# Kernel optimization log

Hardware: AMD Instinct MI355X
Metric: run time of the kernel (lower is better)

## Reference

```python
import jax, jax.numpy as jnp
import numpy as np
from jax import lax

VOL_RANGE = (-40.0, -40.0, -1.0, 40.0, 40.0, 5.4)
VOXEL_SIZE = 0.4
GRID_SHAPE = (200, 200, 16)  # int((hi-lo)/voxel_size) per axis
G = 1024                     # number of gaussians
C = 17                       # feature channels (semantic classes)
MAHA_THRESH = 7.5


def _make_grid_coords():
    # generate_grid(grid_shape, offset=0.5) * voxel_size + vol_range[:3]
    axes = [(jnp.arange(GRID_SHAPE[i], dtype=jnp.float32) + 0.5) * VOXEL_SIZE + VOL_RANGE[i]
            for i in range(3)]
    gx, gy, gz = jnp.meshgrid(*axes, indexing='ij')
    return jnp.stack([gx, gy, gz], axis=-1).reshape(-1, 3)  # [N, 3]


def _quat_to_rotmat(q):
    # q: [..., 4] (w, x, y, z), assumed normalized
    w, x, y, z = q[..., 0], q[..., 1], q[..., 2], q[..., 3]
    R = jnp.stack([
        1 - 2 * (y * y + z * z), 2 * (x * y - w * z), 2 * (x * z + w * y),
        2 * (x * y + w * z), 1 - 2 * (x * x + z * z), 2 * (y * z - w * x),
        2 * (x * z - w * y), 2 * (y * z + w * x), 1 - 2 * (x * x + y * y),
    ], axis=-1)
    return R.reshape(*q.shape[:-1], 3, 3)


def setup_inputs() -> dict:
    key = jax.random.key(0)
    k1, k2, k3, k4, k5 = jax.random.split(key, 5)
    lo = jnp.asarray(VOL_RANGE[:3], dtype=jnp.float32)
    hi = jnp.asarray(VOL_RANGE[3:], dtype=jnp.float32)
    means3d = lo + (hi - lo) * jax.random.uniform(k1, (1, G, 3), dtype=jnp.float32)
    opacities = jax.random.uniform(k2, (1, G, 1), dtype=jnp.float32)
    features = jax.random.normal(k3, (1, G, C), dtype=jnp.float32)
    # SPD covariances: R diag(s^2) R^T with realistic ~1m scales
    quats = jax.random.normal(k4, (1, G, 4), dtype=jnp.float32)
    quats = quats / jnp.linalg.norm(quats, axis=-1, keepdims=True)
    R = _quat_to_rotmat(quats)                                   # [1, G, 3, 3]
    scales = 0.5 + jax.random.uniform(k5, (1, G, 3), dtype=jnp.float32)  # in [0.5, 1.5] m
    covariances = jnp.einsum('bgij,bgj,bgkj->bgik', R, scales ** 2, R)
    return {
        'grid_coords': _make_grid_coords(),
        'means3d': means3d,
        'opacities': opacities,
        'features': features,
        'covariances': covariances,
    }


def _splat_one_batch(coords, means, ops, feats, covs):
    # coords: [N, 3]; means: [G, 3]; ops: [G]; feats: [G, C]; covs: [G, 3, 3]
    N = coords.shape[0]
    c = feats.shape[-1]
    inv_covs = jnp.linalg.inv(covs)  # [G, 3, 3]

    def step(carry, inp):
        dsum, fsum, cnt = carry
        mu, A, op, ft = inp
        diff = coords - mu                                  # [N, 3]
        maha = jnp.einsum('ni,ij,nj->n', diff, A, diff)     # [N]
        mask = maha <= MAHA_THRESH
        w = jnp.where(mask, op * jnp.exp(-0.5 * maha), 0.0)  # density contribution
        mf = mask.astype(coords.dtype)
        dsum = dsum + w
        fsum = fsum + mf[:, None] * (op * ft)[None, :]       # feature contribution
        cnt = cnt + mf
        return (dsum, fsum, cnt), None

    init = (jnp.zeros((N,), coords.dtype),
            jnp.zeros((N, c), coords.dtype),
            jnp.zeros((N,), coords.dtype))
    (dsum, fsum, cnt), _ = lax.scan(step, init, (means, inv_covs, ops, feats))
    # running-mean update in the torch loop == masked mean over gaussians
    denom = jnp.maximum(cnt, 1.0)
    return dsum / denom, fsum / denom[:, None]


def reference(grid_coords, means3d, opacities, features, covariances):
    dens, fts = jax.vmap(_splat_one_batch, in_axes=(None, 0, 0, 0, 0))(
        grid_coords, means3d, opacities[..., 0], features, covariances)
    B = means3d.shape[0]
    dens = dens.reshape(B, *GRID_SHAPE, 1)
    fts = fts.reshape(B, *GRID_SHAPE, features.shape[-1])
    return dens, fts
```

## Files before the change

### kernel.cpp

```cpp
#include <hip/hip_runtime.h>
#include <math.h>

#define G_N 1024
#define C_N 17
#define NX 200
#define NY 200
#define NZ 16
#define N_VOX (NX * NY * NZ)
#define MAHA_T 7.5f
#define CAP 128

__launch_bounds__(256, 2)
__global__ void gv_fused_kernel(const float* __restrict__ means,
                                const float* __restrict__ ops,
                                const float* __restrict__ feats,
                                const float* __restrict__ covs,
                                float* __restrict__ dens_out,
                                float* __restrict__ feat_out) {
    __shared__ __align__(16) char smemA[4 * 64 * C_N * 4];
    __shared__ unsigned short s_list[G_N];
    __shared__ int s_wcnt[4];

    const int tid = threadIdx.x;
    const int wave = tid >> 6;
    const int lane = tid & 63;
    const int bx = blockIdx.x, by = blockIdx.y;

    const float x0 = -40.f + (float)(bx * 8) * 0.4f;
    const float x1 = x0 + 3.2f;
    const float y0 = -40.f + (float)(by * 8) * 0.4f;
    const float y1 = y0 + 3.2f;

    unsigned short* s_stage = (unsigned short*)smemA;
    int base = 0;
#pragma unroll
    for (int r = 0; r < 4; ++r) {
        int g = wave * 256 + r * 64 + lane;
        float mx = means[3 * g], my = means[3 * g + 1], mz = means[3 * g + 2];
        float c00 = covs[9 * g], c11 = covs[9 * g + 4], c22 = covs[9 * g + 8];
        float hx = sqrtf(MAHA_T * c00) * 1.01f + 0.01f;
        float hy = sqrtf(MAHA_T * c11) * 1.01f + 0.01f;
        float hz = sqrtf(MAHA_T * c22) * 1.01f + 0.01f;
        bool hit = (mx - hx <= x1) && (mx + hx >= x0) &&
                   (my - hy <= y1) && (my + hy >= y0) &&
                   (mz - hz <= 5.4f) && (mz + hz >= -1.0f);
        unsigned long long m = __ballot(hit);
        int rank = __popcll(m & ((1ull << lane) - 1ull));
        if (hit) s_stage[wave * 256 + base + rank] = (unsigned short)g;
        base += __popcll(m);
    }
    if (lane == 0) s_wcnt[wave] = base;
    __syncthreads();
    const int c0 = s_wcnt[0], c1 = s_wcnt[1], c2 = s_wcnt[2], c3 = s_wcnt[3];
    const int total = c0 + c1 + c2 + c3;
    int off = 0;
    if (wave > 0) off += c0;
    if (wave > 1) off += c1;
    if (wave > 2) off += c2;
    for (int i = lane; i < base; i += 64)
        s_list[off + i] = s_stage[wave * 256 + i];

    const int z = lane & 15;
    const int yv = lane >> 4;
    const int X0 = bx * 8 + 2 * wave;
    const int X1 = X0 + 1;
    const int Ya = by * 8 + yv;

    float cx0, cx1, cya, cyb, cz;
    {
#pragma clang fp contract(off)
        cx0 = ((float)X0 + 0.5f) * 0.4f + -40.0f;
        cx1 = ((float)X1 + 0.5f) * 0.4f + -40.0f;
        cya = ((float)Ya + 0.5f) * 0.4f + -40.0f;
        cyb = ((float)(Ya + 4) + 0.5f) * 0.4f + -40.0f;
        cz  = ((float)z + 0.5f) * 0.4f + -1.0f;
    }

    float dsa = 0.f, dsb = 0.f, dsc = 0.f, dsd = 0.f;
    float cna = 0.f, cnb = 0.f, cnc = 0.f, cnd = 0.f;
    float fa[C_N], fb[C_N], fc[C_N], fd[C_N];
#pragma unroll
    for (int c = 0; c < C_N; ++c) { fa[c] = 0.f; fb[c] = 0.f; fc[c] = 0.f; fd[c] = 0.f; }

#define ACC(F, DS, CN, MH) { DS = fmaf(q0.w, __expf(-0.5f * (MH)), DS); CN += 1.f; \
    F[0] += q2.z;  F[1] += q2.w;  F[2] += q3.x;  F[3] += q3.y;  F[4] += q3.z; \
    F[5] += q3.w;  F[6] += q4.x;  F[7] += q4.y;  F[8] += q4.z;  F[9] += q4.w; \
    F[10] += q5.x; F[11] += q5.y; F[12] += q5.z; F[13] += q5.w; F[14] += q6.x; \
    F[15] += q6.y; F[16] += q6.z; }

    float4* s_gd = (float4*)smemA;
    for (int cb = 0; cb < total; cb += CAP) {
        const int nc = min(CAP, total - cb);
        __syncthreads();
        if (tid < nc) {
            int g = (int)s_list[cb + tid];
            const float* cv = covs + g * 9;
            double c00 = cv[0], c01 = cv[1], c02 = cv[2];
            double c11 = cv[4], c12 = cv[5], c22 = cv[8];
            double m00 = c11 * c22 - c12 * c12;
            double m01 = c02 * c12 - c01 * c22;
            double m02 = c01 * c12 - c02 * c11;
            double det = c00 * m00 + c01 * m01 + c02 * m02;
            double inv = 1.0 / det;
            float a00 = (float)(m00 * inv);
            float a01 = (float)(m01 * inv);
            float a02 = (float)(m02 * inv);
            float a11 = (float)((c00 * c22 - c02 * c02) * inv);
            float a12 = (float)((c02 * c01 - c00 * c12) * inv);
            float a22 = (float)((c00 * c11 - c01 * c01) * inv);
            float mx = means[3 * g], my = means[3 * g + 1], mz = means[3 * g + 2];
            float op = ops[g];
            const float* ft = feats + g * C_N;
            float4* o = s_gd + tid * 7;
            o[0] = make_float4(mx, my, mz, op);
            o[1] = make_float4(a00, a11, a22, 2.f * a01);
            o[2] = make_float4(2.f * a02, 2.f * a12, op * ft[0], op * ft[1]);
            o[3] = make_float4(op * ft[2], op * ft[3], op * ft[4], op * ft[5]);
            o[4] = make_float4(op * ft[6], op * ft[7], op * ft[8], op * ft[9]);
            o[5] = make_float4(op * ft[10], op * ft[11], op * ft[12], op * ft[13]);
            o[6] = make_float4(op * ft[14], op * ft[15], op * ft[16], 0.f);
        }
        __syncthreads();
        for (int j = 0; j < nc; ++j) {
            const float4* rowp = s_gd + j * 7;
            float4 q0 = rowp[0], q1 = rowp[1], q2 = rowp[2];
            float d0a = cx0 - q0.x, d0b = cx1 - q0.x;
            float d1a = cya - q0.y, d1b = cyb - q0.y;
            float d2  = cz - q0.z;
            float s1 = q2.x * d2;
            float s2 = q2.y * d2;
            float w  = q1.z * d2;
            float sw = d2 * w;
            float va = fmaf(q1.y, d1a, s2);
            float vb = fmaf(q1.y, d1b, s2);
            float ta = fmaf(d1a, va, sw);
            float tb = fmaf(d1b, vb, sw);
            float uaa = fmaf(q1.x, d0a, fmaf(q1.w, d1a, s1));
            float uab = fmaf(q1.x, d0a, fmaf(q1.w, d1b, s1));
            float uba = fmaf(q1.x, d0b, fmaf(q1.w, d1a, s1));
            float ubb = fmaf(q1.x, d0b, fmaf(q1.w, d1b, s1));
            float mA = fmaf(d0a, uaa, ta);
            float mB = fmaf(d0a, uab, tb);
            float mC = fmaf(d0b, uba, ta);
            float mD = fmaf(d0b, ubb, tb);
            bool ha = mA <= MAHA_T, hb = mB <= MAHA_T;
            bool hc = mC <= MAHA_T, hd = mD <= MAHA_T;
            if (ha | hb | hc | hd) {
                float4 q3 = rowp[3], q4 = rowp[4], q5 = rowp[5], q6 = rowp[6];
                if (ha) ACC(fa, dsa, cna, mA);
                if (hb) ACC(fb, dsb, cnb, mB);
                if (hc) ACC(fc, dsc, cnc, mC);
                if (hd) ACC(fd, dsd, cnd, mD);
            }
        }
    }
    __syncthreads();

    float* fw = (float*)(smemA + wave * (64 * C_N * 4));
    const float4* lsrc = (const float4*)fw;

#define EPI(F, DS, CN, XX, HH) { \
    const float rd = 1.f / fmaxf(CN, 1.f); \
    const long nb = (long)16 * ((long)(by * 8 + 4 * (HH)) + 200L * (XX)); \
    dens_out[nb + lane] = DS * rd; \
    _Pragma("unroll") \
    for (int c = 0; c < C_N; ++c) fw[lane * C_N + c] = F[c] * rd; \
    float4* gout = (float4*)(feat_out + nb * C_N); \
    _Pragma("unroll") \
    for (int r = 0; r < 4; ++r) gout[lane + 64 * r] = lsrc[lane + 64 * r]; \
    if (lane < 16) gout[256 + lane] = lsrc[256 + lane]; }

    EPI(fa, dsa, cna, X0, 0);
    EPI(fb, dsb, cnb, X0, 1);
    EPI(fc, dsc, cnc, X1, 0);
    EPI(fd, dsd, cnd, X1, 1);
}

extern "C" void kernel_launch(void* const* d_in, const int* in_sizes, int n_in,
                              void* d_out, int out_size, void* d_ws, size_t ws_size,
                              hipStream_t stream) {
    const float* means3d     = (const float*)d_in[1];
    const float* opacities   = (const float*)d_in[2];
    const float* features    = (const float*)d_in[3];
    const float* covariances = (const float*)d_in[4];

    float* dens_out = (float*)d_out;
    float* feat_out = (float*)d_out + N_VOX;

    dim3 grid(NX / 8, NY / 8);
    gv_fused_kernel<<<grid, 256, 0, stream>>>(means3d, opacities, features,
                                              covariances, dens_out, feat_out);
}
```

Before: 20.45 us.

## Shrink block tile to 4x4 columns with single-wave blocks

Each block now covers a 4x4 xy tile with one 64-lane wave instead of an 8x8 tile with four waves, so per-block gaussian culling is tighter and fewer non-contributing gaussians are evaluated. The Mahalanobis computation is restructured to share y/z terms across four x positions. Culling and inverse-covariance setup are now repeated across four times as many blocks, adding redundant global loads and double-precision work.

```diff
diff --git a/kernel.cpp b/kernel.cpp
--- a/kernel.cpp
+++ b/kernel.cpp
@@ -8,34 +8,30 @@
 #define NZ 16
 #define N_VOX (NX * NY * NZ)
 #define MAHA_T 7.5f
-#define CAP 128
+#define CAP 64
 
-__launch_bounds__(256, 2)
+__launch_bounds__(64, 4)
 __global__ void gv_fused_kernel(const float* __restrict__ means,
                                 const float* __restrict__ ops,
                                 const float* __restrict__ feats,
                                 const float* __restrict__ covs,
                                 float* __restrict__ dens_out,
                                 float* __restrict__ feat_out) {
-    __shared__ __align__(16) char smemA[4 * 64 * C_N * 4];
     __shared__ unsigned short s_list[G_N];
-    __shared__ int s_wcnt[4];
+    __shared__ __align__(16) float4 s_gd[CAP * 7];
+    __shared__ __align__(16) float  s_out[64 * C_N];
 
-    const int tid = threadIdx.x;
-    const int wave = tid >> 6;
-    const int lane = tid & 63;
+    const int lane = threadIdx.x;
     const int bx = blockIdx.x, by = blockIdx.y;
 
-    const float x0 = -40.f + (float)(bx * 8) * 0.4f;
-    const float x1 = x0 + 3.2f;
-    const float y0 = -40.f + (float)(by * 8) * 0.4f;
-    const float y1 = y0 + 3.2f;
+    const float x0 = -40.f + (float)(bx * 4) * 0.4f;
+    const float x1 = x0 + 1.6f;
+    const float y0 = -40.f + (float)(by * 4) * 0.4f;
+    const float y1 = y0 + 1.6f;
 
-    unsigned short* s_stage = (unsigned short*)smemA;
-    int base = 0;
-#pragma unroll
-    for (int r = 0; r < 4; ++r) {
-        int g = wave * 256 + r * 64 + lane;
+    int total = 0;
+    for (int r = 0; r < 16; ++r) {
+        int g = r * 64 + lane;
         float mx = means[3 * g], my = means[3 * g + 1], mz = means[3 * g + 2];
         float c00 = covs[9 * g], c11 = covs[9 * g + 4], c22 = covs[9 * g + 8];
         float hx = sqrtf(MAHA_T * c00) * 1.01f + 0.01f;
@@ -46,33 +42,23 @@
                    (mz - hz <= 5.4f) && (mz + hz >= -1.0f);
         unsigned long long m = __ballot(hit);
         int rank = __popcll(m & ((1ull << lane) - 1ull));
-        if (hit) s_stage[wave * 256 + base + rank] = (unsigned short)g;
-        base += __popcll(m);
+        if (hit) s_list[total + rank] = (unsigned short)g;
+        total += __popcll(m);
     }
-    if (lane == 0) s_wcnt[wave] = base;
-    __syncthreads();
-    const int c0 = s_wcnt[0], c1 = s_wcnt[1], c2 = s_wcnt[2], c3 = s_wcnt[3];
-    const int total = c0 + c1 + c2 + c3;
-    int off = 0;
-    if (wave > 0) off += c0;
-    if (wave > 1) off += c1;
-    if (wave > 2) off += c2;
-    for (int i = lane; i < base; i += 64)
-        s_list[off + i] = s_stage[wave * 256 + i];
 
     const int z = lane & 15;
     const int yv = lane >> 4;
-    const int X0 = bx * 8 + 2 * wave;
-    const int X1 = X0 + 1;
-    const int Ya = by * 8 + yv;
+    const int X0 = bx * 4;
+    const int Y = by * 4 + yv;
 
-    float cx0, cx1, cya, cyb, cz;
+    float cx0, cx1, cx2, cx3, cy, cz;
     {
 #pragma clang fp contract(off)
         cx0 = ((float)X0 + 0.5f) * 0.4f + -40.0f;
-        cx1 = ((float)X1 + 0.5f) * 0.4f + -40.0f;
-        cya = ((float)Ya + 0.5f) * 0.4f + -40.0f;
-        cyb = ((float)(Ya + 4) + 0.5f) * 0.4f + -40.0f;
+        cx1 = ((float)(X0 + 1) + 0.5f) * 0.4f + -40.0f;
+        cx2 = ((float)(X0 + 2) + 0.5f) * 0.4f + -40.0f;
+        cx3 = ((float)(X0 + 3) + 0.5f) * 0.4f + -40.0f;
+        cy  = ((float)Y + 0.5f) * 0.4f + -40.0f;
         cz  = ((float)z + 0.5f) * 0.4f + -1.0f;
     }
 
@@ -88,12 +74,11 @@
     F[10] += q5.x; F[11] += q5.y; F[12] += q5.z; F[13] += q5.w; F[14] += q6.x; \
     F[15] += q6.y; F[16] += q6.z; }
 
-    float4* s_gd = (float4*)smemA;
     for (int cb = 0; cb < total; cb += CAP) {
         const int nc = min(CAP, total - cb);
         __syncthreads();
-        if (tid < nc) {
-            int g = (int)s_list[cb + tid];
+        if (lane < nc) {
+            int g = (int)s_list[cb + lane];
             const float* cv = covs + g * 9;
             double c00 = cv[0], c01 = cv[1], c02 = cv[2];
             double c11 = cv[4], c12 = cv[5], c22 = cv[8];
@@ -111,7 +96,7 @@
             float mx = means[3 * g], my = means[3 * g + 1], mz = means[3 * g + 2];
             float op = ops[g];
             const float* ft = feats + g * C_N;
-            float4* o = s_gd + tid * 7;
+            float4* o = s_gd + lane * 7;
             o[0] = make_float4(mx, my, mz, op);
             o[1] = make_float4(a00, a11, a22, 2.f * a01);
             o[2] = make_float4(2.f * a02, 2.f * a12, op * ft[0], op * ft[1]);
@@ -125,24 +110,21 @@
             const float4* rowp = s_gd + j * 7;
             float4 q0 = rowp[0], q1 = rowp[1], q2 = rowp[2];
             float d0a = cx0 - q0.x, d0b = cx1 - q0.x;
-            float d1a = cya - q0.y, d1b = cyb - q0.y;
-            float d2  = cz - q0.z;
+            float d0c = cx2 - q0.x, d0d = cx3 - q0.x;
+            float d1 = cy - q0.y, d2 = cz - q0.z;
             float s1 = q2.x * d2;
-            float s2 = q2.y * d2;
+            float p  = fmaf(q1.w, d1, s1);
+            float v  = fmaf(q1.y, d1, q2.y * d2);
             float w  = q1.z * d2;
-            float sw = d2 * w;
-            float va = fmaf(q1.y, d1a, s2);
-            float vb = fmaf(q1.y, d1b, s2);
-            float ta = fmaf(d1a, va, sw);
-            float tb = fmaf(d1b, vb, sw);
-            float uaa = fmaf(q1.x, d0a, fmaf(q1.w, d1a, s1));
-            float uab = fmaf(q1.x, d0a, fmaf(q1.w, d1b, s1));
-            float uba = fmaf(q1.x, d0b, fmaf(q1.w, d1a, s1));
-            float ubb = fmaf(q1.x, d0b, fmaf(q1.w, d1b, s1));
-            float mA = fmaf(d0a, uaa, ta);
-            float mB = fmaf(d0a, uab, tb);
-            float mC = fmaf(d0b, uba, ta);
-            float mD = fmaf(d0b, ubb, tb);
+            float t  = fmaf(d1, v, d2 * w);
+            float ua = fmaf(q1.x, d0a, p);
+            float ub = fmaf(q1.x, d0b, p);
+            float uc = fmaf(q1.x, d0c, p);
+            float ud = fmaf(q1.x, d0d, p);
+            float mA = fmaf(d0a, ua, t);
+            float mB = fmaf(d0b, ub, t);
+            float mC = fmaf(d0c, uc, t);
+            float mD = fmaf(d0d, ud, t);
             bool ha = mA <= MAHA_T, hb = mB <= MAHA_T;
             bool hc = mC <= MAHA_T, hd = mD <= MAHA_T;
             if (ha | hb | hc | hd) {
@@ -156,24 +138,24 @@
     }
     __syncthreads();
 
-    float* fw = (float*)(smemA + wave * (64 * C_N * 4));
-    const float4* lsrc = (const float4*)fw;
+    const float4* lsrc = (const float4*)s_out;
 
-#define EPI(F, DS, CN, XX, HH) { \
+#define EPI(F, DS, CN, XI) { \
     const float rd = 1.f / fmaxf(CN, 1.f); \
-    const long nb = (long)16 * ((long)(by * 8 + 4 * (HH)) + 200L * (XX)); \
+    const int nb = 16 * (4 * by + 200 * (X0 + (XI))); \
     dens_out[nb + lane] = DS * rd; \
     _Pragma("unroll") \
-    for (int c = 0; c < C_N; ++c) fw[lane * C_N + c] = F[c] * rd; \
-    float4* gout = (float4*)(feat_out + nb * C_N); \
+    for (int c = 0; c < C_N; ++c) s_out[lane * C_N + c] = F[c] * rd; \
+    float4* gout = (float4*)(feat_out + (long)nb * C_N); \
     _Pragma("unroll") \
     for (int r = 0; r < 4; ++r) gout[lane + 64 * r] = lsrc[lane + 64 * r]; \
-    if (lane < 16) gout[256 + lane] = lsrc[256 + lane]; }
+    if (lane < 16) gout[256 + lane] = lsrc[256 + lane]; \
+    __syncthreads(); }
 
-    EPI(fa, dsa, cna, X0, 0);
-    EPI(fb, dsb, cnb, X0, 1);
-    EPI(fc, dsc, cnc, X1, 0);
-    EPI(fd, dsd, cnd, X1, 1);
+    EPI(fa, dsa, cna, 0);
+    EPI(fb, dsb, cnb, 1);
+    EPI(fc, dsc, cnc, 2);
+    EPI(fd, dsd, cnd, 3);
 }
 
 extern "C" void kernel_launch(void* const* d_in, const int* in_sizes, int n_in,
@@ -187,7 +169,7 @@
     float* dens_out = (float*)d_out;
     float* feat_out = (float*)d_out + N_VOX;
 
-    dim3 grid(NX / 8, NY / 8);
-    gv_fused_kernel<<<grid, 256, 0, stream>>>(means3d, opacities, features,
-                                              covariances, dens_out, feat_out);
+    dim3 grid(NX / 4, NY / 4);
+    gv_fused_kernel<<<grid, 64, 0, stream>>>(means3d, opacities, features,
+                                             covariances, dens_out, feat_out);
 }
```

Measured after the change: 24.65 us. 20.5% more time.

## Precompute per-gaussian params in prep kernel and stream them from global memory

Applied to the files above, without the earlier changes.

Adds a prep kernel that computes inverse covariances, opacity-scaled features and xy bounding boxes (with the z test folded in) once per gaussian, writing them to workspace. The splat kernel now reads the bounding box for culling and streams the gaussian rows from global/L2 with a one-ahead register prefetch, instead of every block recomputing double-precision inverses into shared memory in chunks. This removes the redundant per-block inversion and the chunk barriers. In exchange it costs a second kernel launch, and the inner loop now loads uncached global rows every iteration, which raises register pressure and memory latency.

```diff
diff --git a/kernel.cpp b/kernel.cpp
--- a/kernel.cpp
+++ b/kernel.cpp
@@ -8,13 +8,50 @@
 #define NZ 16
 #define N_VOX (NX * NY * NZ)
 #define MAHA_T 7.5f
-#define CAP 128
+
+
+__global__ void gv_prep_kernel(const float* __restrict__ means,
+                               const float* __restrict__ ops,
+                               const float* __restrict__ feats,
+                               const float* __restrict__ covs,
+                               float4* __restrict__ gp4) {
+    int g = blockIdx.x * blockDim.x + threadIdx.x;
+    if (g >= G_N) return;
+    const float* cv = covs + g * 9;
+    double c00 = cv[0], c01 = cv[1], c02 = cv[2];
+    double c11 = cv[4], c12 = cv[5], c22 = cv[8];
+    double m00 = c11 * c22 - c12 * c12;
+    double m01 = c02 * c12 - c01 * c22;
+    double m02 = c01 * c12 - c02 * c11;
+    double det = c00 * m00 + c01 * m01 + c02 * m02;
+    double inv = 1.0 / det;
+    float a00 = (float)(m00 * inv);
+    float a01 = (float)(m01 * inv);
+    float a02 = (float)(m02 * inv);
+    float a11 = (float)((c00 * c22 - c02 * c02) * inv);
+    float a12 = (float)((c02 * c01 - c00 * c12) * inv);
+    float a22 = (float)((c00 * c11 - c01 * c01) * inv);
+    float mx = means[3 * g], my = means[3 * g + 1], mz = means[3 * g + 2];
+    float op = ops[g];
+    const float* ft = feats + g * C_N;
+    float4* o = gp4 + g * 8;
+    o[0] = make_float4(mx, my, mz, op);
+    o[1] = make_float4(a00, a11, a22, 2.f * a01);
+    o[2] = make_float4(2.f * a02, 2.f * a12, op * ft[0], op * ft[1]);
+    o[3] = make_float4(op * ft[2], op * ft[3], op * ft[4], op * ft[5]);
+    o[4] = make_float4(op * ft[6], op * ft[7], op * ft[8], op * ft[9]);
+    o[5] = make_float4(op * ft[10], op * ft[11], op * ft[12], op * ft[13]);
+    o[6] = make_float4(op * ft[14], op * ft[15], op * ft[16], 0.f);
+    float fc00 = cv[0], fc11 = cv[4], fc22 = cv[8];
+    float hx = sqrtf(MAHA_T * fc00) * 1.01f + 0.01f;
+    float hy = sqrtf(MAHA_T * fc11) * 1.01f + 0.01f;
+    float hz = sqrtf(MAHA_T * fc22) * 1.01f + 0.01f;
+    bool zok = (mz - hz <= 5.4f) && (mz + hz >= -1.0f);
+    o[7] = make_float4(zok ? (mx - hx) : 3.0e38f, mx + hx, my - hy, my + hy);
+}
 
 __launch_bounds__(256, 2)
-__global__ void gv_fused_kernel(const float* __restrict__ means,
-                                const float* __restrict__ ops,
-                                const float* __restrict__ feats,
-                                const float* __restrict__ covs,
+__global__ void gv_splat_kernel(const float4* __restrict__ gp4,
                                 float* __restrict__ dens_out,
                                 float* __restrict__ feat_out) {
     __shared__ __align__(16) char smemA[4 * 64 * C_N * 4];
@@ -36,14 +73,8 @@
 #pragma unroll
     for (int r = 0; r < 4; ++r) {
         int g = wave * 256 + r * 64 + lane;
-        float mx = means[3 * g], my = means[3 * g + 1], mz = means[3 * g + 2];
-        float c00 = covs[9 * g], c11 = covs[9 * g + 4], c22 = covs[9 * g + 8];
-        float hx = sqrtf(MAHA_T * c00) * 1.01f + 0.01f;
-        float hy = sqrtf(MAHA_T * c11) * 1.01f + 0.01f;
-        float hz = sqrtf(MAHA_T * c22) * 1.01f + 0.01f;
-        bool hit = (mx - hx <= x1) && (mx + hx >= x0) &&
-                   (my - hy <= y1) && (my + hy >= y0) &&
-                   (mz - hz <= 5.4f) && (mz + hz >= -1.0f);
+        float4 cb = gp4[g * 8 + 7];
+        bool hit = (cb.x <= x1) && (cb.y >= x0) && (cb.z <= y1) && (cb.w >= y0);
         unsigned long long m = __ballot(hit);
         int rank = __popcll(m & ((1ull << lane) - 1ull));
         if (hit) s_stage[wave * 256 + base + rank] = (unsigned short)g;
@@ -59,6 +90,7 @@
     if (wave > 2) off += c2;
     for (int i = lane; i < base; i += 64)
         s_list[off + i] = s_stage[wave * 256 + i];
+    __syncthreads();
 
     const int z = lane & 15;
     const int yv = lane >> 4;
@@ -88,73 +120,47 @@
     F[10] += q5.x; F[11] += q5.y; F[12] += q5.z; F[13] += q5.w; F[14] += q6.x; \
     F[15] += q6.y; F[16] += q6.z; }
 
-    float4* s_gd = (float4*)smemA;
-    for (int cb = 0; cb < total; cb += CAP) {
-        const int nc = min(CAP, total - cb);
-        __syncthreads();
-        if (tid < nc) {
-            int g = (int)s_list[cb + tid];
-            const float* cv = covs + g * 9;
-            double c00 = cv[0], c01 = cv[1], c02 = cv[2];
-            double c11 = cv[4], c12 = cv[5], c22 = cv[8];
-            double m00 = c11 * c22 - c12 * c12;
-            double m01 = c02 * c12 - c01 * c22;
-            double m02 = c01 * c12 - c02 * c11;
-            double det = c00 * m00 + c01 * m01 + c02 * m02;
-            double inv = 1.0 / det;
-            float a00 = (float)(m00 * inv);
-            float a01 = (float)(m01 * inv);
-            float a02 = (float)(m02 * inv);
-            float a11 = (float)((c00 * c22 - c02 * c02) * inv);
-            float a12 = (float)((c02 * c01 - c00 * c12) * inv);
-            float a22 = (float)((c00 * c11 - c01 * c01) * inv);
-            float mx = means[3 * g], my = means[3 * g + 1], mz = means[3 * g + 2];
-            float op = ops[g];
-            const float* ft = feats + g * C_N;
-            float4* o = s_gd + tid * 7;
-            o[0] = make_float4(mx, my, mz, op);
-            o[1] = make_float4(a00, a11, a22, 2.f * a01);
-            o[2] = make_float4(2.f * a02, 2.f * a12, op * ft[0], op * ft[1]);
-            o[3] = make_float4(op * ft[2], op * ft[3], op * ft[4], op * ft[5]);
-            o[4] = make_float4(op * ft[6], op * ft[7], op * ft[8], op * ft[9]);
-            o[5] = make_float4(op * ft[10], op * ft[11], op * ft[12], op * ft[13]);
-            o[6] = make_float4(op * ft[14], op * ft[15], op * ft[16], 0.f);
+    float4 p0, p1, p2, p3, p4, p5, p6;
+    if (total > 0) {
+        const float4* row = gp4 + (int)s_list[0] * 8;
+        p0 = row[0]; p1 = row[1]; p2 = row[2]; p3 = row[3];
+        p4 = row[4]; p5 = row[5]; p6 = row[6];
+    }
+    for (int j = 0; j < total; ++j) {
+        float4 q0 = p0, q1 = p1, q2 = p2, q3 = p3, q4 = p4, q5 = p5, q6 = p6;
+        if (j + 1 < total) {
+            const float4* row = gp4 + (int)s_list[j + 1] * 8;
+            p0 = row[0]; p1 = row[1]; p2 = row[2]; p3 = row[3];
+            p4 = row[4]; p5 = row[5]; p6 = row[6];
         }
-        __syncthreads();
-        for (int j = 0; j < nc; ++j) {
-            const float4* rowp = s_gd + j * 7;
-            float4 q0 = rowp[0], q1 = rowp[1], q2 = rowp[2];
-            float d0a = cx0 - q0.x, d0b = cx1 - q0.x;
-            float d1a = cya - q0.y, d1b = cyb - q0.y;
-            float d2  = cz - q0.z;
-            float s1 = q2.x * d2;
-            float s2 = q2.y * d2;
-            float w  = q1.z * d2;
-            float sw = d2 * w;
-            float va = fmaf(q1.y, d1a, s2);
-            float vb = fmaf(q1.y, d1b, s2);
-            float ta = fmaf(d1a, va, sw);
-            float tb = fmaf(d1b, vb, sw);
-            float uaa = fmaf(q1.x, d0a, fmaf(q1.w, d1a, s1));
-            float uab = fmaf(q1.x, d0a, fmaf(q1.w, d1b, s1));
-            float uba = fmaf(q1.x, d0b, fmaf(q1.w, d1a, s1));
-            float ubb = fmaf(q1.x, d0b, fmaf(q1.w, d1b, s1));
-            float mA = fmaf(d0a, uaa, ta);
-            float mB = fmaf(d0a, uab, tb);
-            float mC = fmaf(d0b, uba, ta);
-            float mD = fmaf(d0b, ubb, tb);
-            bool ha = mA <= MAHA_T, hb = mB <= MAHA_T;
-            bool hc = mC <= MAHA_T, hd = mD <= MAHA_T;
-            if (ha | hb | hc | hd) {
-                float4 q3 = rowp[3], q4 = rowp[4], q5 = rowp[5], q6 = rowp[6];
-                if (ha) ACC(fa, dsa, cna, mA);
-                if (hb) ACC(fb, dsb, cnb, mB);
-                if (hc) ACC(fc, dsc, cnc, mC);
-                if (hd) ACC(fd, dsd, cnd, mD);
-            }
+        float d0a = cx0 - q0.x, d0b = cx1 - q0.x;
+        float d1a = cya - q0.y, d1b = cyb - q0.y;
+        float d2  = cz - q0.z;
+        float s1 = q2.x * d2;
+        float s2 = q2.y * d2;
+        float w  = q1.z * d2;
+        float sw = d2 * w;
+        float va = fmaf(q1.y, d1a, s2);
+        float vb = fmaf(q1.y, d1b, s2);
+        float ta = fmaf(d1a, va, sw);
+        float tb = fmaf(d1b, vb, sw);
+        float uaa = fmaf(q1.x, d0a, fmaf(q1.w, d1a, s1));
+        float uab = fmaf(q1.x, d0a, fmaf(q1.w, d1b, s1));
+        float uba = fmaf(q1.x, d0b, fmaf(q1.w, d1a, s1));
+        float ubb = fmaf(q1.x, d0b, fmaf(q1.w, d1b, s1));
+        float mA = fmaf(d0a, uaa, ta);
+        float mB = fmaf(d0a, uab, tb);
+        float mC = fmaf(d0b, uba, ta);
+        float mD = fmaf(d0b, ubb, tb);
+        bool ha = mA <= MAHA_T, hb = mB <= MAHA_T;
+        bool hc = mC <= MAHA_T, hd = mD <= MAHA_T;
+        if (ha | hb | hc | hd) {
+            if (ha) ACC(fa, dsa, cna, mA);
+            if (hb) ACC(fb, dsb, cnb, mB);
+            if (hc) ACC(fc, dsc, cnc, mC);
+            if (hd) ACC(fd, dsd, cnd, mD);
         }
     }
-    __syncthreads();
 
     float* fw = (float*)(smemA + wave * (64 * C_N * 4));
     const float4* lsrc = (const float4*)fw;
@@ -186,8 +192,11 @@
 
     float* dens_out = (float*)d_out;
     float* feat_out = (float*)d_out + N_VOX;
-
+    float4* gp4 = (float4*)d_ws;
+
+    gv_prep_kernel<<<(G_N + 255) / 256, 256, 0, stream>>>(means3d, opacities,
+                                                          features, covariances,
+                                                          gp4);
     dim3 grid(NX / 8, NY / 8);
-    gv_fused_kernel<<<grid, 256, 0, stream>>>(means3d, opacities, features,
-                                              covariances, dens_out, feat_out);
+    gv_splat_kernel<<<grid, 256, 0, stream>>>(gp4, dens_out, feat_out);
 }
```

Measured after the change: 26.55 us. 1.3x slower.
